# Kernel tuning notes

Hardware: AMD Instinct MI355X
Metric: run time of the kernel (lower is better)

## Reference

```python
import jax, jax.numpy as jnp
import numpy as np

# ---- hyperparameters (from pars / init_kwargs) ----
ALPHA = 0.9          # synaptic conductance decay (snn.Synaptic alpha)
BETA = 0.8           # membrane decay (snn.Synaptic beta)
BETA_PLUS = 0.9      # pre-synaptic trace decay
BETA_MINUS = 0.9     # post-synaptic trace decay
THRESHOLD = 1.0
W_MIN, W_MAX = 0.0, 1.0
A_PLUS, A_MINUS = 0.008, 0.0008
T, B, IN, N = 350, 128, 784, 400
SPIKE_P = 0.05       # Bernoulli firing probability of the rate-coded input


def setup_inputs() -> dict:
    key = jax.random.key(0)
    k_img, k_w = jax.random.split(key)
    # Poisson/Bernoulli rate-coded MNIST spike train [T, B, IN]
    image = (jax.random.uniform(k_img, (T, B, IN)) < SPIKE_P).astype(jnp.float32)
    # nn.Linear default init U(-1/sqrt(IN), 1/sqrt(IN)) then clamp to [w_min, w_max]
    s = 1.0 / np.sqrt(IN)
    W = jnp.clip(jax.random.uniform(k_w, (N, IN), minval=-s, maxval=s), W_MIN, W_MAX)
    return {"image": image, "W": W}


def reference(image, W):
    """Fused LIF (snntorch Synaptic, reset-by-subtraction) + STDP loop over T steps.

    Returns (W_final, mem_final, syn_final, total_spikes_per_neuron).
    """
    batch = image.shape[1]

    def step(carry, x_t):
        syn, mem, pre_tr, post_tr, W = carry
        # pre-synaptic trace: tr_t = beta_plus * tr_{t-1} + x_t
        pre_tr = BETA_PLUS * pre_tr + x_t                      # [B, IN]
        # linear projection (no bias)
        I_t = jnp.einsum('bi,ni->bn', x_t, W)                  # [B, N]
        # snntorch Synaptic: reset from pre-update mem, subtract mechanism
        reset = (mem > THRESHOLD).astype(mem.dtype)
        syn = ALPHA * syn + I_t
        mem = BETA * mem + syn - reset * THRESHOLD
        spk = (mem > THRESHOLD).astype(mem.dtype)              # [B, N]
        # post-synaptic trace
        post_tr = BETA_MINUS * post_tr + spk
        # STDP: potentiate on post spike x pre trace, depress on pre spike x post trace
        dW = (A_PLUS * jnp.einsum('bn,bi->ni', spk, pre_tr)
              - A_MINUS * jnp.einsum('bn,bi->ni', post_tr, x_t)) / batch
        W = jnp.clip(W + dW, W_MIN, W_MAX)
        return (syn, mem, pre_tr, post_tr, W), spk.sum(axis=0)

    syn0 = jnp.zeros((batch, N), image.dtype)
    mem0 = jnp.zeros((batch, N), image.dtype)
    pre0 = jnp.zeros((batch, IN), image.dtype)
    post0 = jnp.zeros((batch, N), image.dtype)

    (syn, mem, _, _, W_final), spk_counts = jax.lax.scan(
        step, (syn0, mem0, pre0, post0, W), image)
    return W_final, mem, syn, spk_counts.sum(axis=0)
```

## Files before the change

kernel.cpp:

```cpp
#include <hip/hip_runtime.h>
#include <hip/hip_bf16.h>


#define TT    350
#define BB    128
#define INF   784
#define NNEU  400
#define NS    2
#define NTHR  1024
#define LCAP  80

#define ALPHA 0.9f
#define BETA  0.8f
#define BPLUS 0.9f
#define BMIN  0.9f
#define CP    (0.008f/128.0f)
#define CM    (0.0008f/128.0f)

__device__ __forceinline__ float bf2f(__hip_bfloat16 v){ return __bfloat162float(v); }

__global__ void k_pretr(const float* __restrict__ img, __hip_bfloat16* __restrict__ pre){
  int idx = blockIdx.x*blockDim.x + threadIdx.x;
  if (idx >= BB*INF) return;
  float v = 0.f;
  for (int t=0;t<TT;t++){
    v = BPLUS*v + img[(size_t)t*(BB*INF) + idx];
    pre[(size_t)t*(BB*INF) + idx] = __float2bfloat16(v);
  }
}

__global__ void k_S(const __hip_bfloat16* __restrict__ pre, float* __restrict__ S){
  int idx = blockIdx.x*blockDim.x + threadIdx.x;
  if (idx >= TT*INF) return;
  int t = idx / INF, i = idx - t*INF;
  const __hip_bfloat16* p = pre + (size_t)t*(BB*INF) + i;
  float s = 0.f;
  for (int b=0;b<BB;b++) s += bf2f(p[(size_t)b*INF]);
  S[idx] = s;
}

__global__ void k_rowlist(const float* __restrict__ img, unsigned short* __restrict__ lists,
                          int* __restrict__ cnts){
  int gid = blockIdx.x*blockDim.x + threadIdx.x;
  int gw = gid >> 6, lane = gid & 63;
  if (gw >= TT*BB) return;
  __shared__ unsigned short buf[4][LCAP];
  int wl = (threadIdx.x >> 6) & 3;
  const float* p = img + (size_t)gw*INF;
  int cnt = 0;
  for (int wdi=0; wdi<13; wdi++){
    int i = wdi*64 + lane;
    bool a = (i < INF) && (p[i] > 0.f);
    unsigned long long bal = __ballot(a);
    int pos = cnt + __popcll(bal & ((1ull<<lane)-1ull));
    if (a && pos < LCAP) buf[wl][pos] = (unsigned short)i;
    cnt += __popcll(bal);
  }
  for (int k = cnt + lane; k < LCAP; k += 64) buf[wl][k] = (unsigned short)INF;
  if (lane == 0) cnts[gw] = (cnt < LCAP) ? cnt : LCAP;
  if (lane < LCAP/2)
    ((unsigned int*)(lists + (size_t)gw*LCAP))[lane] = ((unsigned int*)buf[wl])[lane];
}

__global__ void k_collist(const float* __restrict__ img, unsigned int* __restrict__ collist){
  int idx = blockIdx.x*blockDim.x + threadIdx.x;
  if (idx >= TT*INF) return;
  int t = idx / INF, i = idx - t*INF;
  const float* p = img + (size_t)t*(BB*INF) + i;
  unsigned long long m0=0, m1=0;
  for (int b=0;b<64;b++) m0 |= ((unsigned long long)(p[(size_t)b*INF]      > 0.f)) << b;
  for (int b=0;b<64;b++) m1 |= ((unsigned long long)(p[(size_t)(64+b)*INF] > 0.f)) << b;
  int cnt = __popcll(m0) + __popcll(m1);
  unsigned int w[8];
  w[0] = (unsigned int)cnt; w[1]=0;w[2]=0;w[3]=0;w[4]=0;w[5]=0;w[6]=0;w[7]=0;
  #pragma unroll
  for (int k=1;k<32;k++){
    int bb;
    if (m0){ bb = __builtin_ctzll(m0); m0 &= m0-1; }
    else if (m1){ bb = 64 + __builtin_ctzll(m1); m1 &= m1-1; }
    else bb = 128;
    w[k>>2] |= ((unsigned int)bb) << ((k&3)*8);
  }
  uint4* dst = (uint4*)(collist + (size_t)idx*8);
  uint4 lo; lo.x=w[0]; lo.y=w[1]; lo.z=w[2]; lo.w=w[3];
  uint4 hi; hi.x=w[4]; hi.y=w[5]; hi.z=w[6]; hi.w=w[7];
  dst[0]=lo; dst[1]=hi;
}

__device__ __forceinline__ float potf(unsigned long long ma, unsigned long long mb,
                                      int pc, float Sv,
                                      const __hip_bfloat16* __restrict__ prt, int c){
  bool direct = (pc <= 64);
  unsigned long long m = direct ? ma : ~ma;
  unsigned long long n = direct ? mb : ~mb;
  float acc = 0.f;
  while (m){ int bb = __builtin_ctzll(m); m &= m-1; acc += bf2f(prt[(size_t)bb*INF + c]); }
  while (n){ int bb = __builtin_ctzll(n); n &= n-1; acc += bf2f(prt[(size_t)(64+bb)*INF + c]); }
  return direct ? acc : (Sv - acc);
}

#define G2(W) { float2 a_ = Wp2[(W) & 0xffffu]; I0 += a_.x; I1 += a_.y; \
                float2 b_ = Wp2[(W) >> 16];     I0 += b_.x; I1 += b_.y; }
#define GATHER8(V) { G2((V).x); G2((V).y); G2((V).z); G2((V).w); }

#define DEP4(W) { float2 p_; \
  p_ = postl[(W) & 0xffu];        d0 += p_.x; d1 += p_.y; \
  p_ = postl[((W)>>8) & 0xffu];   d0 += p_.x; d1 += p_.y; \
  p_ = postl[((W)>>16) & 0xffu];  d0 += p_.x; d1 += p_.y; \
  p_ = postl[(W)>>24];            d0 += p_.x; d1 += p_.y; }

#define DOCOL(c, cl, sv) { \
  float d0=0.f, d1=0.f; \
  unsigned int w0_ = (cl).x; \
  { float2 p_; \
    p_ = postl[(w0_>>8) & 0xffu];  d0 += p_.x; d1 += p_.y; \
    p_ = postl[(w0_>>16) & 0xffu]; d0 += p_.x; d1 += p_.y; \
    p_ = postl[w0_>>24];           d0 += p_.x; d1 += p_.y; } \
  DEP4((cl).y); DEP4((cl).z); DEP4((cl).w); \
  int cc_ = (int)(w0_ & 0xffu); \
  if (cc_ > 15){ \
    uint4 e2_ = *(const uint4*)(collist + ((size_t)t*INF + (c))*8 + 4); \
    DEP4(e2_.x); DEP4(e2_.y); DEP4(e2_.z); DEP4(e2_.w); \
  } \
  float pot0_ = potf(s00, s01, pc0, (sv), prt, (c)); \
  float pot1_ = potf(s10, s11, pc1, (sv), prt, (c)); \
  float2 wv_ = Wp2[(c)]; \
  wv_.x = fminf(fmaxf(wv_.x + CP*pot0_ - CM*d0, 0.f), 1.f); \
  wv_.y = fminf(fmaxf(wv_.y + CP*pot1_ - CM*d1, 0.f), 1.f); \
  Wp2[(c)] = wv_; }

__launch_bounds__(NTHR, 1)
__global__ void k_main(const float* __restrict__ Win,
                       const __hip_bfloat16* __restrict__ pre,
                       const float* __restrict__ S,
                       const unsigned short* __restrict__ lists,
                       const int* __restrict__ cnts,
                       const unsigned int* __restrict__ collist,
                       float* __restrict__ out){
  __shared__ float2 Wp2[800];
  __shared__ float2 postl[132];
  __shared__ unsigned long long smQ[2][2];
  __shared__ float cntS[2];

  const int tid  = threadIdx.x;
  const int lane = tid & 63;
  const int wv   = tid >> 6;
  const int q    = lane >> 3;
  const int b    = (wv << 3) | (lane & 7);
  const int n0   = blockIdx.x * NS;

  if (tid < 800){
    float2 w;
    w.x = (tid < INF) ? Win[(size_t)n0*INF + tid] : 0.f;
    w.y = (tid < INF) ? Win[(size_t)(n0+1)*INF + tid] : 0.f;
    Wp2[tid] = w;
  }
  if (tid < 132){ postl[tid].x = 0.f; postl[tid].y = 0.f; }
  if (tid < 2) cntS[tid] = 0.f;

  const int  c0   = tid;
  const bool hasc = (c0 < INF);

  float syn0=0.f, mem0=0.f, syn1=0.f, mem1=0.f, sc0=0.f, sc1=0.f;

  const unsigned short* lp0 = lists + ((size_t)b)*LCAP + (size_t)q*8;
  uint4 lA = *(const uint4*)lp0;
  int cn = cnts[b];
  uint4 cl0; cl0.x=0;cl0.y=0;cl0.z=0;cl0.w=0;
  float sv0 = 0.f;
  if (hasc){ cl0 = *(const uint4*)(collist + (size_t)c0*8); sv0 = S[c0]; }

  for (int t=0; t<TT; t++){
    __syncthreads();
    float I0 = 0.f, I1 = 0.f;
    GATHER8(lA);
    if (cn > 64 + q*8){
      uint4 lC = *(const uint4*)(lists + ((size_t)t*BB + b)*LCAP + 64 + (size_t)q*8);
      GATHER8(lC);
    }
    int tn = (t+1 < TT) ? t+1 : TT-1;
    uint4 lAn = *(const uint4*)(lists + ((size_t)tn*BB + b)*LCAP + (size_t)q*8);
    int cnn = cnts[tn*BB + b];
    uint4 cl0n = cl0; float sv0n = sv0;
    if (hasc){
      cl0n = *(const uint4*)(collist + ((size_t)tn*INF + c0)*8);
      sv0n = S[tn*INF + c0];
    }

    I0 += __shfl_xor(I0, 8); I0 += __shfl_xor(I0, 16); I0 += __shfl_xor(I0, 32);
    I1 += __shfl_xor(I1, 8); I1 += __shfl_xor(I1, 16); I1 += __shfl_xor(I1, 32);

    float r0 = (mem0 > 1.f) ? 1.f : 0.f;
    syn0 = ALPHA*syn0 + I0;
    mem0 = BETA*mem0 + syn0 - r0;
    float s0 = (mem0 > 1.f) ? 1.f : 0.f;
    float r1 = (mem1 > 1.f) ? 1.f : 0.f;
    syn1 = ALPHA*syn1 + I1;
    mem1 = BETA*mem1 + syn1 - r1;
    float s1 = (mem1 > 1.f) ? 1.f : 0.f;
    unsigned long long bal0 = __ballot(s0 > 0.5f);
    unsigned long long bal1 = __ballot(s1 > 0.5f);
    if (q == 0){
      sc0 += s0; sc1 += s1;
      float2 pv = postl[b];
      pv.x = BMIN*pv.x + s0;
      pv.y = BMIN*pv.y + s1;
      postl[b] = pv;
    }
    if (lane == 0){
      ((unsigned char*)smQ)[wv]      = (unsigned char)(bal0 & 0xffu);
      ((unsigned char*)smQ)[16 + wv] = (unsigned char)(bal1 & 0xffu);
    }
    __syncthreads();

    unsigned long long s00 = smQ[0][0], s01 = smQ[0][1];
    unsigned long long s10 = smQ[1][0], s11 = smQ[1][1];
    int pc0 = __popcll(s00) + __popcll(s01);
    int pc1 = __popcll(s10) + __popcll(s11);
    const __hip_bfloat16* prt = pre + (size_t)t*(BB*INF);
    if (hasc) DOCOL(c0, cl0, sv0)

    lA=lAn; cn=cnn; cl0=cl0n; sv0=sv0n;
  }

  __syncthreads();
  if (tid < INF){
    float2 wvv = Wp2[tid];
    out[(size_t)n0*INF + tid]       = wvv.x;
    out[(size_t)(n0+1)*INF + tid]   = wvv.y;
  }
  if (q == 0){
    out[(size_t)NNEU*INF + (size_t)b*NNEU + n0]                        = mem0;
    out[(size_t)NNEU*INF + (size_t)b*NNEU + n0 + 1]                    = mem1;
    out[(size_t)NNEU*INF + (size_t)BB*NNEU + (size_t)b*NNEU + n0]      = syn0;
    out[(size_t)NNEU*INF + (size_t)BB*NNEU + (size_t)b*NNEU + n0 + 1]  = syn1;
    atomicAdd(&cntS[0], sc0);
    atomicAdd(&cntS[1], sc1);
  }
  __syncthreads();
  if (tid < 2) out[(size_t)NNEU*INF + 2*(size_t)BB*NNEU + n0 + tid] = cntS[tid];
}

extern "C" void kernel_launch(void* const* d_in, const int* in_sizes, int n_in,
                              void* d_out, int out_size, void* d_ws, size_t ws_size,
                              hipStream_t stream) {
  const float* img = (const float*)d_in[0];
  const float* W   = (const float*)d_in[1];
  float* out = (float*)d_out;

  char* ws = (char*)d_ws;
  __hip_bfloat16* pre  = (__hip_bfloat16*)ws;
  float*          S    = (float*)(ws + 70246400);
  unsigned short* lst  = (unsigned short*)(ws + 71344000);
  int*            cnts = (int*)(ws + 78512000);
  unsigned int*   coll = (unsigned int*)(ws + 78691200);

  k_pretr  <<<(BB*INF + 255)/256, 256, 0, stream>>>(img, pre);
  k_S      <<<(TT*INF + 255)/256, 256, 0, stream>>>(pre, S);
  k_rowlist<<<(TT*BB*64)/256,     256, 0, stream>>>(img, lst, cnts);
  k_collist<<<(TT*INF + 255)/256, 256, 0, stream>>>(img, coll);
  k_main   <<<NNEU/NS, NTHR, 0, stream>>>(W, pre, S, lst, cnts, coll, out);
}
```

Measured before the change: 718.8 us.

## Merge mask kernels, add uniform-spike fast STDP path, custom barriers

Replaces the separate row-list and column-list kernels with one per-timestep kernel that builds ballot bitmasks in shared memory once and derives both lists from them. In the main loop it adds a fast path for steps where all or no batch rows spike for each neuron and the post traces are uniform across the batch. In that case the STDP update becomes a closed form using the column sum and column count, which skips the per-column gathers. It also pre-scales list indices to byte offsets, replaces __syncthreads with a lightweight lgkmcnt-wait barrier, and moves the loop barrier to the end of each iteration. The added uniformity check and extra barrier cost some work every step, and the fast path depends on whether spiking is saturated or silent.

```diff
diff --git a/kernel.cpp b/kernel.cpp
--- a/kernel.cpp
+++ b/kernel.cpp
@@ -18,6 +18,12 @@
 #define CM    (0.0008f/128.0f)
 
 __device__ __forceinline__ float bf2f(__hip_bfloat16 v){ return __bfloat162float(v); }
+
+__device__ __forceinline__ void barx(){
+  asm volatile("s_waitcnt lgkmcnt(0)" ::: "memory");
+  __builtin_amdgcn_s_barrier();
+  __builtin_amdgcn_sched_barrier(0);
+}
 
 __global__ void k_pretr(const float* __restrict__ img, __hip_bfloat16* __restrict__ pre){
   int idx = blockIdx.x*blockDim.x + threadIdx.x;
@@ -39,52 +45,64 @@
   S[idx] = s;
 }
 
-__global__ void k_rowlist(const float* __restrict__ img, unsigned short* __restrict__ lists,
-                          int* __restrict__ cnts){
-  int gid = blockIdx.x*blockDim.x + threadIdx.x;
-  int gw = gid >> 6, lane = gid & 63;
-  if (gw >= TT*BB) return;
-  __shared__ unsigned short buf[4][LCAP];
-  int wl = (threadIdx.x >> 6) & 3;
-  const float* p = img + (size_t)gw*INF;
-  int cnt = 0;
-  for (int wdi=0; wdi<13; wdi++){
-    int i = wdi*64 + lane;
-    bool a = (i < INF) && (p[i] > 0.f);
-    unsigned long long bal = __ballot(a);
-    int pos = cnt + __popcll(bal & ((1ull<<lane)-1ull));
-    if (a && pos < LCAP) buf[wl][pos] = (unsigned short)i;
-    cnt += __popcll(bal);
-  }
-  for (int k = cnt + lane; k < LCAP; k += 64) buf[wl][k] = (unsigned short)INF;
-  if (lane == 0) cnts[gw] = (cnt < LCAP) ? cnt : LCAP;
-  if (lane < LCAP/2)
-    ((unsigned int*)(lists + (size_t)gw*LCAP))[lane] = ((unsigned int*)buf[wl])[lane];
-}
-
-__global__ void k_collist(const float* __restrict__ img, unsigned int* __restrict__ collist){
-  int idx = blockIdx.x*blockDim.x + threadIdx.x;
-  if (idx >= TT*INF) return;
-  int t = idx / INF, i = idx - t*INF;
-  const float* p = img + (size_t)t*(BB*INF) + i;
-  unsigned long long m0=0, m1=0;
-  for (int b=0;b<64;b++) m0 |= ((unsigned long long)(p[(size_t)b*INF]      > 0.f)) << b;
-  for (int b=0;b<64;b++) m1 |= ((unsigned long long)(p[(size_t)(64+b)*INF] > 0.f)) << b;
-  int cnt = __popcll(m0) + __popcll(m1);
-  unsigned int w[8];
-  w[0] = (unsigned int)cnt; w[1]=0;w[2]=0;w[3]=0;w[4]=0;w[5]=0;w[6]=0;w[7]=0;
-  #pragma unroll
-  for (int k=1;k<32;k++){
-    int bb;
-    if (m0){ bb = __builtin_ctzll(m0); m0 &= m0-1; }
-    else if (m1){ bb = 64 + __builtin_ctzll(m1); m1 &= m1-1; }
-    else bb = 128;
-    w[k>>2] |= ((unsigned int)bb) << ((k&3)*8);
-  }
-  uint4* dst = (uint4*)(collist + (size_t)idx*8);
-  uint4 lo; lo.x=w[0]; lo.y=w[1]; lo.z=w[2]; lo.w=w[3];
-  uint4 hi; hi.x=w[4]; hi.y=w[5]; hi.z=w[6]; hi.w=w[7];
-  dst[0]=lo; dst[1]=hi;
+__global__ void k_masks(const float* __restrict__ img,
+                        unsigned short* __restrict__ lists,
+                        int* __restrict__ cnts,
+                        unsigned int* __restrict__ collist){
+  __shared__ unsigned long long rowbits[BB][13];
+  __shared__ unsigned short buf[16][LCAP];
+  const int t = blockIdx.x;
+  const int tid = threadIdx.x, lane = tid & 63, w = tid >> 6;
+  const float* base = img + (size_t)t*(BB*INF);
+
+  for (int r8=0; r8<8; r8++){
+    int r = w*8 + r8;
+    const float* p = base + (size_t)r*INF;
+    for (int c=0;c<13;c++){
+      int i = c*64 + lane;
+      bool a = (i < INF) && (p[i] > 0.f);
+      unsigned long long bal = __ballot(a);
+      if (lane == 0) rowbits[r][c] = bal;
+    }
+  }
+  for (int r8=0; r8<8; r8++){
+    int r = w*8 + r8;
+    int cnt = 0;
+    for (int c=0;c<13;c++){
+      unsigned long long word = rowbits[r][c];
+      int i = c*64 + lane;
+      bool a = (word >> lane) & 1ull;
+      int pos = cnt + __popcll(word & ((1ull<<lane)-1ull));
+      if (a && pos < LCAP) buf[w][pos] = (unsigned short)(i<<3);
+      cnt += __popcll(word);
+    }
+    for (int k = cnt + lane; k < LCAP; k += 64) buf[w][k] = (unsigned short)(INF<<3);
+    if (lane == 0) cnts[t*BB + r] = (cnt < LCAP) ? cnt : LCAP;
+    if (lane < LCAP/2)
+      ((unsigned int*)(lists + (size_t)(t*BB + r)*LCAP))[lane] = ((unsigned int*)buf[w])[lane];
+  }
+  __syncthreads();
+  if (tid < INF){
+    int wsel = tid >> 6, bit = tid & 63;
+    unsigned long long m0=0, m1=0;
+    for (int b=0;b<64;b++) m0 |= ((rowbits[b][wsel]    >> bit) & 1ull) << b;
+    for (int b=0;b<64;b++) m1 |= ((rowbits[64+b][wsel] >> bit) & 1ull) << b;
+    int cnt = __popcll(m0) + __popcll(m1);
+    unsigned int wd[8];
+    wd[0] = (unsigned int)cnt; wd[1]=0;wd[2]=0;wd[3]=0;wd[4]=0;wd[5]=0;wd[6]=0;wd[7]=0;
+    #pragma unroll
+    for (int k=1;k<32;k++){
+      int bb;
+      if (m0){ bb = __builtin_ctzll(m0); m0 &= m0-1; }
+      else if (m1){ bb = 64 + __builtin_ctzll(m1); m1 &= m1-1; }
+      else bb = 128;
+      wd[k>>2] |= ((unsigned int)bb) << ((k&3)*8);
+    }
+    uint4* dst = (uint4*)(collist + ((size_t)t*INF + tid)*8);
+    uint4 lo; lo.x=wd[0]; lo.y=wd[1]; lo.z=wd[2]; lo.w=wd[3];
+    uint4 hi; hi.x=wd[4]; hi.y=wd[5]; hi.z=wd[6]; hi.w=wd[7];
+    dst[0]=lo; dst[1]=hi;
+  }
 }
 
 __device__ __forceinline__ float potf(unsigned long long ma, unsigned long long mb,
@@ -99,8 +117,8 @@
   return direct ? acc : (Sv - acc);
 }
 
-#define G2(W) { float2 a_ = Wp2[(W) & 0xffffu]; I0 += a_.x; I1 += a_.y; \
-                float2 b_ = Wp2[(W) >> 16];     I0 += b_.x; I1 += b_.y; }
+#define G2(W) { float2 a_ = *(const float2*)((const char*)&Wp2[0] + ((W) & 0xffffu)); I0 += a_.x; I1 += a_.y; \
+                float2 b_ = *(const float2*)((const char*)&Wp2[0] + ((W) >> 16));     I0 += b_.x; I1 += b_.y; }
 #define GATHER8(V) { G2((V).x); G2((V).y); G2((V).z); G2((V).w); }
 
 #define DEP4(W) { float2 p_; \
@@ -141,6 +159,8 @@
   __shared__ float2 postl[132];
   __shared__ unsigned long long smQ[2][2];
   __shared__ float cntS[2];
+  __shared__ float2 postCb[2];
+  __shared__ int    unifb[2];
 
   const int tid  = threadIdx.x;
   const int lane = tid & 63;
@@ -157,21 +177,25 @@
   }
   if (tid < 132){ postl[tid].x = 0.f; postl[tid].y = 0.f; }
   if (tid < 2) cntS[tid] = 0.f;
+  if (tid == 0){
+    postCb[0].x = 0.f; postCb[0].y = 0.f; unifb[0] = 1;
+    postCb[1].x = 0.f; postCb[1].y = 0.f; unifb[1] = 1;
+  }
 
   const int  c0   = tid;
   const bool hasc = (c0 < INF);
 
   float syn0=0.f, mem0=0.f, syn1=0.f, mem1=0.f, sc0=0.f, sc1=0.f;
 
-  const unsigned short* lp0 = lists + ((size_t)b)*LCAP + (size_t)q*8;
-  uint4 lA = *(const uint4*)lp0;
+  uint4 lA = *(const uint4*)(lists + ((size_t)b)*LCAP + (size_t)q*8);
   int cn = cnts[b];
   uint4 cl0; cl0.x=0;cl0.y=0;cl0.z=0;cl0.w=0;
   float sv0 = 0.f;
   if (hasc){ cl0 = *(const uint4*)(collist + (size_t)c0*8); sv0 = S[c0]; }
 
+  __syncthreads();
+
   for (int t=0; t<TT; t++){
-    __syncthreads();
     float I0 = 0.f, I1 = 0.f;
     GATHER8(lA);
     if (cn > 64 + q*8){
@@ -211,16 +235,47 @@
       ((unsigned char*)smQ)[wv]      = (unsigned char)(bal0 & 0xffu);
       ((unsigned char*)smQ)[16 + wv] = (unsigned char)(bal1 & 0xffu);
     }
-    __syncthreads();
+    barx();
 
     unsigned long long s00 = smQ[0][0], s01 = smQ[0][1];
     unsigned long long s10 = smQ[1][0], s11 = smQ[1][1];
-    int pc0 = __popcll(s00) + __popcll(s01);
-    int pc1 = __popcll(s10) + __popcll(s11);
-    const __hip_bfloat16* prt = pre + (size_t)t*(BB*INF);
-    if (hasc) DOCOL(c0, cl0, sv0)
+    bool full0 = (s00 & s01) == ~0ull, none0 = (s00 | s01) == 0ull;
+    bool full1 = (s10 & s11) == ~0ull, none1 = (s10 | s11) == 0ull;
+    int   fastOK = unifb[t & 1] && (full0 || none0) && (full1 || none1);
+    float2 pC = postCb[t & 1];
+
+    if (wv == 13){
+      float2 a0 = postl[lane], a1 = postl[64 + lane];
+      float2 rr = postl[0];
+      bool eq = (a0.x==rr.x) && (a0.y==rr.y) && (a1.x==rr.x) && (a1.y==rr.y);
+      unsigned long long bal = __ballot(eq);
+      if (lane == 0){ unifb[(t+1) & 1] = (bal == ~0ull); postCb[(t+1) & 1] = rr; }
+    }
+
+    if (fastOK){
+      if (hasc){
+        float sa0 = full0 ? 1.f : 0.f, sa1 = full1 ? 1.f : 0.f;
+        float cur0 = BMIN*pC.x + sa0, cur1 = BMIN*pC.y + sa1;
+        bool allzero = none0 && none1 && (pC.x == 0.f) && (pC.y == 0.f);
+        if (!allzero){
+          float cc  = (float)(int)(cl0.x & 0xffu);
+          float pot0 = full0 ? sv0 : 0.f;
+          float pot1 = full1 ? sv0 : 0.f;
+          float2 wv_ = Wp2[c0];
+          wv_.x = fminf(fmaxf(wv_.x + CP*pot0 - CM*(cur0*cc), 0.f), 1.f);
+          wv_.y = fminf(fmaxf(wv_.y + CP*pot1 - CM*(cur1*cc), 0.f), 1.f);
+          Wp2[c0] = wv_;
+        }
+      }
+    } else {
+      int pc0 = __popcll(s00) + __popcll(s01);
+      int pc1 = __popcll(s10) + __popcll(s11);
+      const __hip_bfloat16* prt = pre + (size_t)t*(BB*INF);
+      if (hasc) DOCOL(c0, cl0, sv0)
+    }
 
     lA=lAn; cn=cnn; cl0=cl0n; sv0=sv0n;
+    barx();
   }
 
   __syncthreads();
@@ -255,9 +310,8 @@
   int*            cnts = (int*)(ws + 78512000);
   unsigned int*   coll = (unsigned int*)(ws + 78691200);
 
-  k_pretr  <<<(BB*INF + 255)/256, 256, 0, stream>>>(img, pre);
-  k_S      <<<(TT*INF + 255)/256, 256, 0, stream>>>(pre, S);
-  k_rowlist<<<(TT*BB*64)/256,     256, 0, stream>>>(img, lst, cnts);
-  k_collist<<<(TT*INF + 255)/256, 256, 0, stream>>>(img, coll);
-  k_main   <<<NNEU/NS, NTHR, 0, stream>>>(W, pre, S, lst, cnts, coll, out);
-}
+  k_pretr<<<(BB*INF + 255)/256, 256, 0, stream>>>(img, pre);
+  k_masks<<<TT, NTHR, 0, stream>>>(img, lst, cnts, coll);
+  k_S    <<<(TT*INF + 255)/256, 256, 0, stream>>>(pre, S);
+  k_main <<<NNEU/NS, NTHR, 0, stream>>>(W, pre, S, lst, cnts, coll, out);
+}
```

Result: no change. 727.5 us (+1.2%).
